# Performance work log

Measured on AMD Instinct MI355X. Metric: run time of the kernel, lower is better.

Reference implementation:

```python
import jax, jax.numpy as jnp
import numpy as np

N0, N1, N2 = 331776, 36864, 4096   # src nodes block0, mid nodes, final items
E0, E1, EP = 294912, 32768, 4096   # edges block0, block1, pos/neg edges
F_RAW, D, H = 128, 256, 512        # raw feat dim, hidden_dims_sum, 2*hidden
N_NODES = 1000000                  # global graph node count (scorer bias)


def setup_inputs() -> dict:
    key = jax.random.key(0)
    ks = jax.random.split(key, 24)
    ri = lambda k, n, hi: jax.random.randint(k, (n,), 0, hi, dtype=jnp.int64 if False else jnp.int32).astype(jnp.int32)
    s = 0.05
    return {
        "feat0": jax.random.normal(ks[0], (N0, F_RAW), jnp.float32),
        "feat_dst": jax.random.normal(ks[1], (N2, F_RAW), jnp.float32),
        "weights0": jax.random.uniform(ks[2], (E0,), jnp.float32),
        "weights1": jax.random.uniform(ks[3], (E1,), jnp.float32),
        "W_proj": jax.random.normal(ks[4], (F_RAW, D), jnp.float32) * s,
        "b_proj": jnp.zeros((D,), jnp.float32),
        "Q1": jax.random.normal(ks[5], (D, H), jnp.float32) * s,
        "bq1": jnp.zeros((H,), jnp.float32),
        "W1": jax.random.normal(ks[6], (D + H, D), jnp.float32) * s,
        "bw1": jnp.zeros((D,), jnp.float32),
        "Q2": jax.random.normal(ks[7], (D, H), jnp.float32) * s,
        "bq2": jnp.zeros((H,), jnp.float32),
        "W2": jax.random.normal(ks[8], (D + H, D), jnp.float32) * s,
        "bw2": jnp.zeros((D,), jnp.float32),
        "bias": jnp.zeros((N_NODES,), jnp.float32),
        "block0_src": ri(ks[9], E0, N0),
        "block0_dst": ri(ks[10], E0, N1),
        "block1_src": ri(ks[11], E1, N1),
        "block1_dst": ri(ks[12], E1, N2),
        "pos_src": ri(ks[13], EP, N2),
        "pos_dst": ri(ks[14], EP, N2),
        "neg_src": ri(ks[15], EP, N2),
        "neg_dst": ri(ks[16], EP, N2),
        "nid": ri(ks[17], N2, N_NODES),
    }


def _l2norm(z):
    n = jnp.linalg.norm(z, axis=1, keepdims=True)
    return z / jnp.where(n == 0, 1.0, n)


def _sage_conv(h_src, h_dst, src, dst, w, Q, bq, W, bw, n_dst):
    # WeightedSAGEConv (dropout omitted: eval-mode deterministic reference)
    n = jax.nn.relu(h_src @ Q + bq)                                   # [N_src, H]
    m = jax.ops.segment_sum(n[src] * w[:, None], dst, num_segments=n_dst)
    ws = jnp.clip(jax.ops.segment_sum(w, dst, num_segments=n_dst), 1.0, None)
    z = jax.nn.relu(jnp.concatenate([m / ws[:, None], h_dst], axis=1) @ W + bw)
    return _l2norm(z)


def _score(h, src, dst, nid, bias):
    # ItemToItemScorer: u_dot_v + src/dst node bias
    return jnp.sum(h[src] * h[dst], axis=1) + bias[nid[src]] + bias[nid[dst]]


def reference(feat0, feat_dst, weights0, weights1, W_proj, b_proj, Q1, bq1, W1, bw1,
              Q2, bq2, W2, bw2, bias, block0_src, block0_dst, block1_src, block1_dst,
              pos_src, pos_dst, neg_src, neg_dst, nid):
    h = feat0 @ W_proj + b_proj                                         # LinearProjector
    h = _sage_conv(h, h[:N1], block0_src, block0_dst, weights0, Q1, bq1, W1, bw1, N1)
    h = _sage_conv(h, h[:N2], block1_src, block1_dst, weights1, Q2, bq2, W2, bw2, N2)
    h_item = (feat_dst @ W_proj + b_proj) + h                           # get_repr skip-add
    pos_score = _score(h_item, pos_src, pos_dst, nid, bias)
    neg_score = _score(h_item, neg_src, neg_dst, nid, bias)
    return (pos_score, neg_score)
```

## Files before the change

kernel.cpp:

```cpp
#include <hip/hip_runtime.h>
#include <hip/hip_bf16.h>

typedef __hip_bfloat16 bf16;
typedef __attribute__((ext_vector_type(8))) short frag8;
typedef __attribute__((ext_vector_type(4))) float f32x4;

#define N0c 331776
#define N1c 36864
#define N2c 4096
#define E0c 294912
#define E1c 32768

__device__ __forceinline__ float bfbits2f(unsigned short b) {
    union { unsigned u; float f; } x; x.u = ((unsigned)b) << 16; return x.f;
}
__device__ __forceinline__ unsigned short f2bfbits(float f) {
    bf16 h = __float2bfloat16(f);
    return *reinterpret_cast<unsigned short*>(&h);
}
__device__ __forceinline__ void load4f(const float* p, float* o) {
    const float4 v = *reinterpret_cast<const float4*>(p);
    o[0] = v.x; o[1] = v.y; o[2] = v.z; o[3] = v.w;
}
__device__ __forceinline__ ushort4 pack4(float4 v) {
    ushort4 o; o.x = f2bfbits(v.x); o.y = f2bfbits(v.y);
    o.z = f2bfbits(v.z); o.w = f2bfbits(v.w); return o;
}
__device__ __forceinline__ void store_c(float* p, float v) { *p = v; }
__device__ __forceinline__ void store_c(bf16* p, float v)  { *p = __float2bfloat16(v); }
__device__ __forceinline__ f32x4 zero4() {
    f32x4 z; z[0] = 0.f; z[1] = 0.f; z[2] = 0.f; z[3] = 0.f; return z;
}
__device__ __forceinline__ f32x4 mfma16(frag8 a, frag8 b, f32x4 c) {
    return __builtin_amdgcn_mfma_f32_16x16x32_bf16(a, b, c, 0, 0, 0);
}

__global__ __launch_bounds__(256) void transpose_bf16(
    const float* __restrict__ src, bf16* __restrict__ dst, int K, int N)
{
    const int idx = blockIdx.x * 256 + threadIdx.x;
    if (idx >= K * N) return;
    const int k = idx / N, n = idx - k * N;
    dst[(size_t)n * K + k] = __float2bfloat16(src[idx]);
}

template<typename TC>
__global__ __launch_bounds__(256) void gemm_mfma_proj(
    const float* __restrict__ A, const bf16* __restrict__ WpT,
    const float* __restrict__ bp, TC* __restrict__ C)
{
    __shared__ bf16 Xs[64 * 136];

    const int tid = threadIdx.x;
    const int lane = tid & 63, wave = tid >> 6;
    const int row0 = blockIdx.x * 64;

    {
        const int r = tid >> 2, q = tid & 3;
        const float* ar = A + (size_t)(row0 + r) * 128 + q * 32;
        bf16* xr = Xs + r * 136 + q * 32;
        #pragma unroll
        for (int i = 0; i < 8; ++i)
            *reinterpret_cast<ushort4*>(xr + i * 4) =
                pack4(*reinterpret_cast<const float4*>(ar + i * 4));
    }
    __syncthreads();

    const int lr = lane & 15;
    const int lk = (lane >> 4) * 8;
    const int lm4 = (lane >> 4) * 4;

    f32x4 acc[4][4];
    #pragma unroll
    for (int mi = 0; mi < 4; ++mi)
        #pragma unroll
        for (int ni = 0; ni < 4; ++ni) acc[mi][ni] = zero4();

    #pragma unroll
    for (int kk = 0; kk < 4; ++kk) {
        frag8 a[4], b[4];
        #pragma unroll
        for (int mi = 0; mi < 4; ++mi)
            a[mi] = *reinterpret_cast<const frag8*>(&Xs[(mi * 16 + lr) * 136 + kk * 32 + lk]);
        #pragma unroll
        for (int ni = 0; ni < 4; ++ni)
            b[ni] = *reinterpret_cast<const frag8*>(
                WpT + (size_t)(wave * 64 + ni * 16 + lr) * 128 + kk * 32 + lk);
        #pragma unroll
        for (int mi = 0; mi < 4; ++mi)
            #pragma unroll
            for (int ni = 0; ni < 4; ++ni)
                acc[mi][ni] = mfma16(a[mi], b[ni], acc[mi][ni]);
    }

    #pragma unroll
    for (int ni = 0; ni < 4; ++ni) {
        const int c = wave * 64 + ni * 16 + lr;
        const float bb = bp[c];
        #pragma unroll
        for (int mi = 0; mi < 4; ++mi)
            #pragma unroll
            for (int i = 0; i < 4; ++i)
                store_c(C + (size_t)(row0 + mi * 16 + lm4 + i) * 256 + c,
                        acc[mi][ni][i] + bb);
    }
}

template<typename TC>
__global__ __launch_bounds__(256) void gemm_mfma_concat(
    const float* __restrict__ m, const float* __restrict__ wsum,
    const bf16* __restrict__ hdst, const bf16* __restrict__ WT,
    const float* __restrict__ bias, TC* __restrict__ C)
{
    __shared__ bf16 As[64 * 136];

    const int tid = threadIdx.x;
    const int lane = tid & 63, wave = tid >> 6;
    const int row0 = blockIdx.x * 64;
    const int r = tid >> 2, q = tid & 3;
    const float inv = 1.f / fmaxf(wsum[row0 + r], 1.f);

    const int lr = lane & 15;
    const int lk = (lane >> 4) * 8;
    const int lm4 = (lane >> 4) * 4;

    f32x4 acc[4][4];
    #pragma unroll
    for (int mi = 0; mi < 4; ++mi)
        #pragma unroll
        for (int ni = 0; ni < 4; ++ni) acc[mi][ni] = zero4();

    #pragma unroll
    for (int ch = 0; ch < 6; ++ch) {
        bf16* xr = As + r * 136 + q * 32;
        if (ch < 4) {
            const float* srcp = m + (size_t)(row0 + r) * 512 + ch * 128 + q * 32;
            #pragma unroll
            for (int i = 0; i < 8; ++i) {
                float4 v = *reinterpret_cast<const float4*>(srcp + i * 4);
                v.x *= inv; v.y *= inv; v.z *= inv; v.w *= inv;
                *reinterpret_cast<ushort4*>(xr + i * 4) = pack4(v);
            }
        } else {
            const bf16* srcp = hdst + (size_t)(row0 + r) * 256 + (ch - 4) * 128 + q * 32;
            #pragma unroll
            for (int i = 0; i < 8; ++i)
                *reinterpret_cast<ushort4*>(xr + i * 4) =
                    *reinterpret_cast<const ushort4*>(srcp + i * 4);
        }
        __syncthreads();

        #pragma unroll
        for (int kk = 0; kk < 4; ++kk) {
            frag8 a[4], b[4];
            #pragma unroll
            for (int mi = 0; mi < 4; ++mi)
                a[mi] = *reinterpret_cast<const frag8*>(&As[(mi * 16 + lr) * 136 + kk * 32 + lk]);
            #pragma unroll
            for (int ni = 0; ni < 4; ++ni)
                b[ni] = *reinterpret_cast<const frag8*>(
                    WT + (size_t)(wave * 64 + ni * 16 + lr) * 768 + ch * 128 + kk * 32 + lk);
            #pragma unroll
            for (int mi = 0; mi < 4; ++mi)
                #pragma unroll
                for (int ni = 0; ni < 4; ++ni)
                    acc[mi][ni] = mfma16(a[mi], b[ni], acc[mi][ni]);
        }
        __syncthreads();
    }

    #pragma unroll
    for (int ni = 0; ni < 4; ++ni) {
        const int c = wave * 64 + ni * 16 + lr;
        const float bb = bias[c];
        #pragma unroll
        for (int mi = 0; mi < 4; ++mi)
            #pragma unroll
            for (int i = 0; i < 4; ++i)
                store_c(C + (size_t)(row0 + mi * 16 + lm4 + i) * 256 + c,
                        fmaxf(acc[mi][ni][i] + bb, 0.f));
    }
}

__global__ __launch_bounds__(256) void edge1_mfma(
    const float* __restrict__ feat0, const bf16* __restrict__ WpT,
    const float* __restrict__ bp, const bf16* __restrict__ Q1T,
    const float* __restrict__ bq1,
    const int* __restrict__ src, const int* __restrict__ dst,
    const float* __restrict__ w,
    float* __restrict__ mout, float* __restrict__ wsum)
{
    __shared__ bf16 Xs[64 * 136];
    __shared__ bf16 Hs[64 * 264];
    __shared__ int   dsts[64];
    __shared__ float wts[64];

    const int tid = threadIdx.x;
    const int lane = tid & 63, wave = tid >> 6;
    const size_t e0 = (size_t)blockIdx.x * 64;

    if (tid < 64) { dsts[tid] = dst[e0 + tid]; wts[tid] = w[e0 + tid]; }

    {
        const int r = tid >> 2, q = tid & 3;
        const int s = src[e0 + r];
        const float* fr = feat0 + (size_t)s * 128 + q * 32;
        bf16* xr = Xs + r * 136 + q * 32;
        #pragma unroll
        for (int i = 0; i < 8; ++i)
            *reinterpret_cast<ushort4*>(xr + i * 4) =
                pack4(*reinterpret_cast<const float4*>(fr + i * 4));
    }
    __syncthreads();

    const int lr = lane & 15;
    const int lk = (lane >> 4) * 8;
    const int lm4 = (lane >> 4) * 4;

    {
        f32x4 acc[4][4];
        #pragma unroll
        for (int mi = 0; mi < 4; ++mi)
            #pragma unroll
            for (int ni = 0; ni < 4; ++ni) acc[mi][ni] = zero4();

        #pragma unroll
        for (int kk = 0; kk < 4; ++kk) {
            frag8 a[4], b[4];
            #pragma unroll
            for (int mi = 0; mi < 4; ++mi)
                a[mi] = *reinterpret_cast<const frag8*>(&Xs[(mi * 16 + lr) * 136 + kk * 32 + lk]);
            #pragma unroll
            for (int ni = 0; ni < 4; ++ni)
                b[ni] = *reinterpret_cast<const frag8*>(
                    WpT + (size_t)(wave * 64 + ni * 16 + lr) * 128 + kk * 32 + lk);
            #pragma unroll
            for (int mi = 0; mi < 4; ++mi)
                #pragma unroll
                for (int ni = 0; ni < 4; ++ni)
                    acc[mi][ni] = mfma16(a[mi], b[ni], acc[mi][ni]);
        }
        #pragma unroll
        for (int ni = 0; ni < 4; ++ni) {
            const int c = wave * 64 + ni * 16 + lr;
            const float bb = bp[c];
            #pragma unroll
            for (int mi = 0; mi < 4; ++mi)
                #pragma unroll
                for (int i = 0; i < 4; ++i)
                    Hs[(mi * 16 + lm4 + i) * 264 + c] =
                        __float2bfloat16(acc[mi][ni][i] + bb);
        }
    }
    __syncthreads();

    #pragma unroll
    for (int pass = 0; pass < 2; ++pass) {
        const int nc0 = wave * 128 + pass * 64;
        f32x4 acc[4][4];
        #pragma unroll
        for (int mi = 0; mi < 4; ++mi)
            #pragma unroll
            for (int ni = 0; ni < 4; ++ni) acc[mi][ni] = zero4();

        #pragma unroll
        for (int kk = 0; kk < 8; ++kk) {
            frag8 a[4], b[4];
            #pragma unroll
            for (int mi = 0; mi < 4; ++mi)
                a[mi] = *reinterpret_cast<const frag8*>(&Hs[(mi * 16 + lr) * 264 + kk * 32 + lk]);
            #pragma unroll
            for (int ni = 0; ni < 4; ++ni)
                b[ni] = *reinterpret_cast<const frag8*>(
                    Q1T + (size_t)(nc0 + ni * 16 + lr) * 256 + kk * 32 + lk);
            #pragma unroll
            for (int mi = 0; mi < 4; ++mi)
                #pragma unroll
                for (int ni = 0; ni < 4; ++ni)
                    acc[mi][ni] = mfma16(a[mi], b[ni], acc[mi][ni]);
        }
        #pragma unroll
        for (int ni = 0; ni < 4; ++ni) {
            const int c = nc0 + ni * 16 + lr;
            const float bb = bq1[c];
            #pragma unroll
            for (int mi = 0; mi < 4; ++mi)
                #pragma unroll
                for (int i = 0; i < 4; ++i) {
                    const int row = mi * 16 + lm4 + i;
                    const float val = fmaxf(acc[mi][ni][i] + bb, 0.f) * wts[row];
                    atomicAdd(&mout[(size_t)dsts[row] * 512 + c], val);
                }
        }
    }
    if (tid < 64) atomicAdd(&wsum[dsts[tid]], wts[tid]);
}

__global__ __launch_bounds__(256) void edge2_mfma(
    const bf16* __restrict__ zn, const bf16* __restrict__ Q2T,
    const float* __restrict__ bq2,
    const int* __restrict__ src, const int* __restrict__ dst,
    const float* __restrict__ w,
    float* __restrict__ mout, float* __restrict__ wsum)
{
    __shared__ bf16 Zs[64 * 264];
    __shared__ int   dsts[64];
    __shared__ float wts[64];

    const int tid = threadIdx.x;
    const int lane = tid & 63, wave = tid >> 6;
    const size_t e0 = (size_t)blockIdx.x * 64;

    if (tid < 64) { dsts[tid] = dst[e0 + tid]; wts[tid] = w[e0 + tid]; }

    {
        const int r = tid >> 2, q = tid & 3;
        const int s = src[e0 + r];
        const bf16* zr = zn + (size_t)s * 256 + q * 64;
        bf16* zo = Zs + r * 264 + q * 64;
        #pragma unroll
        for (int i = 0; i < 16; ++i)
            *reinterpret_cast<ushort4*>(zo + i * 4) =
                *reinterpret_cast<const ushort4*>(zr + i * 4);
    }
    __syncthreads();

    const int lr = lane & 15;
    const int lk = (lane >> 4) * 8;
    const int lm4 = (lane >> 4) * 4;

    #pragma unroll
    for (int pass = 0; pass < 2; ++pass) {
        const int nc0 = wave * 128 + pass * 64;
        f32x4 acc[4][4];
        #pragma unroll
        for (int mi = 0; mi < 4; ++mi)
            #pragma unroll
            for (int ni = 0; ni < 4; ++ni) acc[mi][ni] = zero4();

        #pragma unroll
        for (int kk = 0; kk < 8; ++kk) {
            frag8 a[4], b[4];
            #pragma unroll
            for (int mi = 0; mi < 4; ++mi)
                a[mi] = *reinterpret_cast<const frag8*>(&Zs[(mi * 16 + lr) * 264 + kk * 32 + lk]);
            #pragma unroll
            for (int ni = 0; ni < 4; ++ni)
                b[ni] = *reinterpret_cast<const frag8*>(
                    Q2T + (size_t)(nc0 + ni * 16 + lr) * 256 + kk * 32 + lk);
            #pragma unroll
            for (int mi = 0; mi < 4; ++mi)
                #pragma unroll
                for (int ni = 0; ni < 4; ++ni)
                    acc[mi][ni] = mfma16(a[mi], b[ni], acc[mi][ni]);
        }
        #pragma unroll
        for (int ni = 0; ni < 4; ++ni) {
            const int c = nc0 + ni * 16 + lr;
            const float bb = bq2[c];
            #pragma unroll
            for (int mi = 0; mi < 4; ++mi)
                #pragma unroll
                for (int i = 0; i < 4; ++i) {
                    const int row = mi * 16 + lm4 + i;
                    const float val = fmaxf(acc[mi][ni][i] + bb, 0.f) * wts[row];
                    atomicAdd(&mout[(size_t)dsts[row] * 512 + c], val);
                }
        }
    }
    if (tid < 64) atomicAdd(&wsum[dsts[tid]], wts[tid]);
}

__global__ __launch_bounds__(256) void l2norm_kernel(
    const bf16* __restrict__ Z, bf16* __restrict__ out, int rows)
{
    const int wave = threadIdx.x >> 6, lane = threadIdx.x & 63;
    const int row = blockIdx.x * 4 + wave;
    if (row >= rows) return;
    const ushort4 u = *reinterpret_cast<const ushort4*>(Z + (size_t)row * 256 + lane * 4);
    float v[4] = { bfbits2f(u.x), bfbits2f(u.y), bfbits2f(u.z), bfbits2f(u.w) };
    float ss = v[0]*v[0] + v[1]*v[1] + v[2]*v[2] + v[3]*v[3];
    #pragma unroll
    for (int off = 32; off; off >>= 1) ss += __shfl_xor(ss, off, 64);
    const float scale = (ss == 0.f) ? 1.f : (1.f / sqrtf(ss));
    ushort4 o;
    o.x = f2bfbits(v[0]*scale); o.y = f2bfbits(v[1]*scale);
    o.z = f2bfbits(v[2]*scale); o.w = f2bfbits(v[3]*scale);
    *reinterpret_cast<ushort4*>(out + (size_t)row * 256 + lane * 4) = o;
}

__global__ __launch_bounds__(256) void l2norm_add_kernel(
    const float* __restrict__ Z, const float* __restrict__ P,
    float* __restrict__ out, int rows)
{
    const int wave = threadIdx.x >> 6, lane = threadIdx.x & 63;
    const int row = blockIdx.x * 4 + wave;
    if (row >= rows) return;
    float v[4];
    load4f(Z + (size_t)row * 256 + lane * 4, v);
    float ss = v[0]*v[0] + v[1]*v[1] + v[2]*v[2] + v[3]*v[3];
    #pragma unroll
    for (int off = 32; off; off >>= 1) ss += __shfl_xor(ss, off, 64);
    const float scale = (ss == 0.f) ? 1.f : (1.f / sqrtf(ss));
    float p[4];
    load4f(P + (size_t)row * 256 + lane * 4, p);
    float4 o;
    o.x = p[0] + v[0]*scale; o.y = p[1] + v[1]*scale;
    o.z = p[2] + v[2]*scale; o.w = p[3] + v[3]*scale;
    *reinterpret_cast<float4*>(out + (size_t)row * 256 + lane * 4) = o;
}

__global__ __launch_bounds__(256) void score_kernel(
    const float* __restrict__ h,
    const int* __restrict__ ps, const int* __restrict__ pdi,
    const int* __restrict__ ns, const int* __restrict__ nd,
    const int* __restrict__ nid, const float* __restrict__ bias,
    float* __restrict__ out)
{
    const int wave = threadIdx.x >> 6, lane = threadIdx.x & 63;
    const int e = blockIdx.x * 4 + wave;
    const int ei = e & 4095;
    const int s = (e < 4096) ? ps[ei] : ns[ei];
    const int d = (e < 4096) ? pdi[ei] : nd[ei];
    float a[4], b[4];
    load4f(h + (size_t)s * 256 + lane * 4, a);
    load4f(h + (size_t)d * 256 + lane * 4, b);
    float dot = a[0]*b[0] + a[1]*b[1] + a[2]*b[2] + a[3]*b[3];
    #pragma unroll
    for (int off = 32; off; off >>= 1) dot += __shfl_xor(dot, off, 64);
    if (lane == 0)
        out[e] = dot + bias[nid[s]] + bias[nid[d]];
}

extern "C" void kernel_launch(void* const* d_in, const int* in_sizes, int n_in,
                              void* d_out, int out_size, void* d_ws, size_t ws_size,
                              hipStream_t stream)
{
    const float* feat0    = (const float*)d_in[0];
    const float* feat_dst = (const float*)d_in[1];
    const float* weights0 = (const float*)d_in[2];
    const float* weights1 = (const float*)d_in[3];
    const float* W_proj   = (const float*)d_in[4];
    const float* b_proj   = (const float*)d_in[5];
    const float* Q1       = (const float*)d_in[6];
    const float* bq1      = (const float*)d_in[7];
    const float* W1       = (const float*)d_in[8];
    const float* bw1      = (const float*)d_in[9];
    const float* Q2       = (const float*)d_in[10];
    const float* bq2      = (const float*)d_in[11];
    const float* W2       = (const float*)d_in[12];
    const float* bw2      = (const float*)d_in[13];
    const float* biasN    = (const float*)d_in[14];
    const int* b0s = (const int*)d_in[15];
    const int* b0d = (const int*)d_in[16];
    const int* b1s = (const int*)d_in[17];
    const int* b1d = (const int*)d_in[18];
    const int* pos_src = (const int*)d_in[19];
    const int* pos_dst = (const int*)d_in[20];
    const int* neg_src = (const int*)d_in[21];
    const int* neg_dst = (const int*)d_in[22];
    const int* nid     = (const int*)d_in[23];

    char* ws = (char*)d_ws;
    size_t off = 0;
    auto alloc = [&](size_t bytes) -> void* {
        void* p = ws + off; off += (bytes + 255) & ~(size_t)255; return p;
    };
    float* m1    = (float*)alloc((size_t)N1c * 512 * 4);
    bf16*  h1dst = (bf16*) alloc((size_t)N1c * 256 * 2);
    bf16*  z1b   = (bf16*) alloc((size_t)N1c * 256 * 2);
    float* ws0   = (float*)alloc((size_t)N1c * 4);
    bf16*  WpT   = (bf16*) alloc((size_t)256 * 128 * 2);
    bf16*  Q1T   = (bf16*) alloc((size_t)512 * 256 * 2);
    bf16*  Q2T   = (bf16*) alloc((size_t)512 * 256 * 2);
    bf16*  W1T   = (bf16*) alloc((size_t)256 * 768 * 2);
    bf16*  W2T   = (bf16*) alloc((size_t)256 * 768 * 2);

    char* r1 = (char*)m1;
    float* m2     = (float*)r1;
    float* ws1    = (float*)(r1 + (size_t)N2c * 512 * 4);
    float* z2     = (float*)(r1 + (size_t)N2c * 512 * 4 + 65536);
    float* pdbuf  = z2 + (size_t)N2c * 256;
    float* h_item = pdbuf + (size_t)N2c * 256;
    bf16* z1n = h1dst;

    transpose_bf16<<<(128*256 + 255)/256, 256, 0, stream>>>(W_proj, WpT, 128, 256);
    transpose_bf16<<<(256*512 + 255)/256, 256, 0, stream>>>(Q1, Q1T, 256, 512);
    transpose_bf16<<<(256*512 + 255)/256, 256, 0, stream>>>(Q2, Q2T, 256, 512);
    transpose_bf16<<<(768*256 + 255)/256, 256, 0, stream>>>(W1, W1T, 768, 256);
    transpose_bf16<<<(768*256 + 255)/256, 256, 0, stream>>>(W2, W2T, 768, 256);

    hipMemsetAsync(m1,  0, (size_t)N1c * 512 * 4, stream);
    hipMemsetAsync(ws0, 0, (size_t)N1c * 4,       stream);

    gemm_mfma_proj<bf16><<<N1c/64, 256, 0, stream>>>(feat0, WpT, b_proj, h1dst);

    edge1_mfma<<<E0c/64, 256, 0, stream>>>(
        feat0, WpT, b_proj, Q1T, bq1, b0s, b0d, weights0, m1, ws0);

    gemm_mfma_concat<bf16><<<N1c/64, 256, 0, stream>>>(
        m1, ws0, h1dst, W1T, bw1, z1b);

    l2norm_kernel<<<N1c/4, 256, 0, stream>>>(z1b, z1n, N1c);

    hipMemsetAsync(m2,  0, (size_t)N2c * 512 * 4, stream);
    hipMemsetAsync(ws1, 0, (size_t)N2c * 4,       stream);

    edge2_mfma<<<E1c/64, 256, 0, stream>>>(
        z1n, Q2T, bq2, b1s, b1d, weights1, m2, ws1);

    gemm_mfma_concat<float><<<N2c/64, 256, 0, stream>>>(
        m2, ws1, z1n, W2T, bw2, z2);

    gemm_mfma_proj<float><<<N2c/64, 256, 0, stream>>>(feat_dst, WpT, b_proj, pdbuf);

    l2norm_add_kernel<<<N2c/4, 256, 0, stream>>>(z2, pdbuf, h_item, N2c);

    score_kernel<<<2048, 256, 0, stream>>>(
        h_item, pos_src, pos_dst, neg_src, neg_dst, nid, biasN, (float*)d_out);
}
```

Measured before the change: 741.5 us.

## Replace atomic scatter aggregation with CSR sort-by-destination and segmented reduction

Builds a destination-sorted permutation (histogram, scan, fill) for each block's edges. The edge kernels now write per-edge bf16 messages to a buffer, and a per-destination reduce kernel sums them and divides by the weight sum, which replaces the float atomics into m. Layer 1 now projects all N0 source nodes once with a GEMM instead of recomputing the projection for every edge. The cost is a large per-edge message buffer, a single-block scan, extra launches, and bf16 rounding of the messages and the mean.

```diff
diff --git a/kernel.cpp b/kernel.cpp
--- a/kernel.cpp
+++ b/kernel.cpp
@@ -44,6 +44,48 @@
     dst[(size_t)n * K + k] = __float2bfloat16(src[idx]);
 }
 
+__global__ __launch_bounds__(256) void hist_kernel(
+    const int* __restrict__ dst, int* __restrict__ cnt, int E)
+{
+    const int e = blockIdx.x * 256 + threadIdx.x;
+    if (e < E) atomicAdd(&cnt[dst[e]], 1);
+}
+
+__global__ __launch_bounds__(256) void scan_kernel(
+    const int* __restrict__ cnt, int* __restrict__ base, int n)
+{
+    __shared__ int ps[256];
+    const int t = threadIdx.x;
+    const int chunk = (n + 255) >> 8;
+    const int lo = t * chunk;
+    const int hi = (lo + chunk < n) ? lo + chunk : n;
+    int s = 0;
+    for (int i = lo; i < hi; ++i) s += cnt[i];
+    ps[t] = s;
+    __syncthreads();
+    for (int off = 1; off < 256; off <<= 1) {
+        int v = (t >= off) ? ps[t - off] : 0;
+        __syncthreads();
+        ps[t] += v;
+        __syncthreads();
+    }
+    int run = ps[t] - s;
+    for (int i = lo; i < hi; ++i) { base[i] = run; run += cnt[i]; }
+    if (t == 255) base[n] = ps[255];
+}
+
+__global__ __launch_bounds__(256) void fill_kernel(
+    const int* __restrict__ dst, const int* __restrict__ base,
+    int* __restrict__ cursor, int* __restrict__ perm, int E)
+{
+    const int e = blockIdx.x * 256 + threadIdx.x;
+    if (e < E) {
+        const int d = dst[e];
+        const int p = base[d] + atomicAdd(&cursor[d], 1);
+        perm[p] = e;
+    }
+}
+
 template<typename TC>
 __global__ __launch_bounds__(256) void gemm_mfma_proj(
     const float* __restrict__ A, const bf16* __restrict__ WpT,
@@ -106,11 +148,113 @@
     }
 }
 
+__global__ __launch_bounds__(256) void edge_csr(
+    const bf16* __restrict__ zn, const bf16* __restrict__ QT,
+    const float* __restrict__ bq,
+    const int* __restrict__ perm, const int* __restrict__ src,
+    const float* __restrict__ w,
+    bf16* __restrict__ nbuf)
+{
+    __shared__ bf16 Zs[64 * 264];
+    __shared__ int   srcs[64];
+    __shared__ float wts[64];
+
+    const int tid = threadIdx.x;
+    const int lane = tid & 63, wave = tid >> 6;
+    const size_t p0 = (size_t)blockIdx.x * 64;
+
+    if (tid < 64) {
+        const int e = perm[p0 + tid];
+        srcs[tid] = src[e];
+        wts[tid]  = w[e];
+    }
+    __syncthreads();
+
+    {
+        const int r = tid >> 2, q = tid & 3;
+        const bf16* zr = zn + (size_t)srcs[r] * 256 + q * 64;
+        bf16* zo = Zs + r * 264 + q * 64;
+        #pragma unroll
+        for (int i = 0; i < 16; ++i)
+            *reinterpret_cast<ushort4*>(zo + i * 4) =
+                *reinterpret_cast<const ushort4*>(zr + i * 4);
+    }
+    __syncthreads();
+
+    const int lr = lane & 15;
+    const int lk = (lane >> 4) * 8;
+    const int lm4 = (lane >> 4) * 4;
+
+    #pragma unroll
+    for (int pass = 0; pass < 2; ++pass) {
+        const int nc0 = wave * 128 + pass * 64;
+        f32x4 acc[4][4];
+        #pragma unroll
+        for (int mi = 0; mi < 4; ++mi)
+            #pragma unroll
+            for (int ni = 0; ni < 4; ++ni) acc[mi][ni] = zero4();
+
+        #pragma unroll
+        for (int kk = 0; kk < 8; ++kk) {
+            frag8 a[4], b[4];
+            #pragma unroll
+            for (int mi = 0; mi < 4; ++mi)
+                a[mi] = *reinterpret_cast<const frag8*>(&Zs[(mi * 16 + lr) * 264 + kk * 32 + lk]);
+            #pragma unroll
+            for (int ni = 0; ni < 4; ++ni)
+                b[ni] = *reinterpret_cast<const frag8*>(
+                    QT + (size_t)(nc0 + ni * 16 + lr) * 256 + kk * 32 + lk);
+            #pragma unroll
+            for (int mi = 0; mi < 4; ++mi)
+                #pragma unroll
+                for (int ni = 0; ni < 4; ++ni)
+                    acc[mi][ni] = mfma16(a[mi], b[ni], acc[mi][ni]);
+        }
+        #pragma unroll
+        for (int ni = 0; ni < 4; ++ni) {
+            const int c = nc0 + ni * 16 + lr;
+            const float bb = bq[c];
+            #pragma unroll
+            for (int mi = 0; mi < 4; ++mi)
+                #pragma unroll
+                for (int i = 0; i < 4; ++i) {
+                    const int row = mi * 16 + lm4 + i;
+                    const float val = fmaxf(acc[mi][ni][i] + bb, 0.f) * wts[row];
+                    nbuf[(p0 + row) * 512 + c] = __float2bfloat16(val);
+                }
+        }
+    }
+}
+
+__global__ __launch_bounds__(256) void reduce_csr(
+    const bf16* __restrict__ nbuf, const int* __restrict__ base,
+    const int* __restrict__ perm, const float* __restrict__ w,
+    bf16* __restrict__ mout)
+{
+    const int d = blockIdx.x;
+    const int lo = base[d], hi = base[d + 1];
+    __shared__ float s_inv;
+    if (threadIdx.x == 0) {
+        float s = 0.f;
+        for (int k = lo; k < hi; ++k) s += w[perm[k]];
+        s_inv = 1.f / fmaxf(s, 1.f);
+    }
+    __syncthreads();
+    const int c = threadIdx.x * 2;
+    float a0 = 0.f, a1 = 0.f;
+    for (int k = lo; k < hi; ++k) {
+        const ushort2 u = *reinterpret_cast<const ushort2*>(nbuf + (size_t)k * 512 + c);
+        a0 += bfbits2f(u.x); a1 += bfbits2f(u.y);
+    }
+    ushort2 o; o.x = f2bfbits(a0 * s_inv); o.y = f2bfbits(a1 * s_inv);
+    *reinterpret_cast<ushort2*>(mout + (size_t)d * 512 + c) = o;
+}
+
 template<typename TC>
 __global__ __launch_bounds__(256) void gemm_mfma_concat(
-    const float* __restrict__ m, const float* __restrict__ wsum,
-    const bf16* __restrict__ hdst, const bf16* __restrict__ WT,
-    const float* __restrict__ bias, TC* __restrict__ C)
+    const bf16* __restrict__ m, const bf16* __restrict__ hdst,
+    const bf16* __restrict__ WT, const float* __restrict__ bias,
+    TC* __restrict__ C)
 {
     __shared__ bf16 As[64 * 136];
 
@@ -118,7 +262,6 @@
     const int lane = tid & 63, wave = tid >> 6;
     const int row0 = blockIdx.x * 64;
     const int r = tid >> 2, q = tid & 3;
-    const float inv = 1.f / fmaxf(wsum[row0 + r], 1.f);
 
     const int lr = lane & 15;
     const int lk = (lane >> 4) * 8;
@@ -133,21 +276,13 @@
     #pragma unroll
     for (int ch = 0; ch < 6; ++ch) {
         bf16* xr = As + r * 136 + q * 32;
-        if (ch < 4) {
-            const float* srcp = m + (size_t)(row0 + r) * 512 + ch * 128 + q * 32;
-            #pragma unroll
-            for (int i = 0; i < 8; ++i) {
-                float4 v = *reinterpret_cast<const float4*>(srcp + i * 4);
-                v.x *= inv; v.y *= inv; v.z *= inv; v.w *= inv;
-                *reinterpret_cast<ushort4*>(xr + i * 4) = pack4(v);
-            }
-        } else {
-            const bf16* srcp = hdst + (size_t)(row0 + r) * 256 + (ch - 4) * 128 + q * 32;
-            #pragma unroll
-            for (int i = 0; i < 8; ++i)
-                *reinterpret_cast<ushort4*>(xr + i * 4) =
-                    *reinterpret_cast<const ushort4*>(srcp + i * 4);
-        }
+        const bf16* srcp = (ch < 4)
+            ? m    + (size_t)(row0 + r) * 512 + ch * 128 + q * 32
+            : hdst + (size_t)(row0 + r) * 256 + (ch - 4) * 128 + q * 32;
+        #pragma unroll
+        for (int i = 0; i < 8; ++i)
+            *reinterpret_cast<ushort4*>(xr + i * 4) =
+                *reinterpret_cast<const ushort4*>(srcp + i * 4);
         __syncthreads();
 
         #pragma unroll
@@ -180,195 +315,6 @@
                 store_c(C + (size_t)(row0 + mi * 16 + lm4 + i) * 256 + c,
                         fmaxf(acc[mi][ni][i] + bb, 0.f));
     }
-}
-
-__global__ __launch_bounds__(256) void edge1_mfma(
-    const float* __restrict__ feat0, const bf16* __restrict__ WpT,
-    const float* __restrict__ bp, const bf16* __restrict__ Q1T,
-    const float* __restrict__ bq1,
-    const int* __restrict__ src, const int* __restrict__ dst,
-    const float* __restrict__ w,
-    float* __restrict__ mout, float* __restrict__ wsum)
-{
-    __shared__ bf16 Xs[64 * 136];
-    __shared__ bf16 Hs[64 * 264];
-    __shared__ int   dsts[64];
-    __shared__ float wts[64];
-
-    const int tid = threadIdx.x;
-    const int lane = tid & 63, wave = tid >> 6;
-    const size_t e0 = (size_t)blockIdx.x * 64;
-
-    if (tid < 64) { dsts[tid] = dst[e0 + tid]; wts[tid] = w[e0 + tid]; }
-
-    {
-        const int r = tid >> 2, q = tid & 3;
-        const int s = src[e0 + r];
-        const float* fr = feat0 + (size_t)s * 128 + q * 32;
-        bf16* xr = Xs + r * 136 + q * 32;
-        #pragma unroll
-        for (int i = 0; i < 8; ++i)
-            *reinterpret_cast<ushort4*>(xr + i * 4) =
-                pack4(*reinterpret_cast<const float4*>(fr + i * 4));
-    }
-    __syncthreads();
-
-    const int lr = lane & 15;
-    const int lk = (lane >> 4) * 8;
-    const int lm4 = (lane >> 4) * 4;
-
-    {
-        f32x4 acc[4][4];
-        #pragma unroll
-        for (int mi = 0; mi < 4; ++mi)
-            #pragma unroll
-            for (int ni = 0; ni < 4; ++ni) acc[mi][ni] = zero4();
-
-        #pragma unroll
-        for (int kk = 0; kk < 4; ++kk) {
-            frag8 a[4], b[4];
-            #pragma unroll
-            for (int mi = 0; mi < 4; ++mi)
-                a[mi] = *reinterpret_cast<const frag8*>(&Xs[(mi * 16 + lr) * 136 + kk * 32 + lk]);
-            #pragma unroll
-            for (int ni = 0; ni < 4; ++ni)
-                b[ni] = *reinterpret_cast<const frag8*>(
-                    WpT + (size_t)(wave * 64 + ni * 16 + lr) * 128 + kk * 32 + lk);
-            #pragma unroll
-            for (int mi = 0; mi < 4; ++mi)
-                #pragma unroll
-                for (int ni = 0; ni < 4; ++ni)
-                    acc[mi][ni] = mfma16(a[mi], b[ni], acc[mi][ni]);
-        }
-        #pragma unroll
-        for (int ni = 0; ni < 4; ++ni) {
-            const int c = wave * 64 + ni * 16 + lr;
-            const float bb = bp[c];
-            #pragma unroll
-            for (int mi = 0; mi < 4; ++mi)
-                #pragma unroll
-                for (int i = 0; i < 4; ++i)
-                    Hs[(mi * 16 + lm4 + i) * 264 + c] =
-                        __float2bfloat16(acc[mi][ni][i] + bb);
-        }
-    }
-    __syncthreads();
-
-    #pragma unroll
-    for (int pass = 0; pass < 2; ++pass) {
-        const int nc0 = wave * 128 + pass * 64;
-        f32x4 acc[4][4];
-        #pragma unroll
-        for (int mi = 0; mi < 4; ++mi)
-            #pragma unroll
-            for (int ni = 0; ni < 4; ++ni) acc[mi][ni] = zero4();
-
-        #pragma unroll
-        for (int kk = 0; kk < 8; ++kk) {
-            frag8 a[4], b[4];
-            #pragma unroll
-            for (int mi = 0; mi < 4; ++mi)
-                a[mi] = *reinterpret_cast<const frag8*>(&Hs[(mi * 16 + lr) * 264 + kk * 32 + lk]);
-            #pragma unroll
-            for (int ni = 0; ni < 4; ++ni)
-                b[ni] = *reinterpret_cast<const frag8*>(
-                    Q1T + (size_t)(nc0 + ni * 16 + lr) * 256 + kk * 32 + lk);
-            #pragma unroll
-            for (int mi = 0; mi < 4; ++mi)
-                #pragma unroll
-                for (int ni = 0; ni < 4; ++ni)
-                    acc[mi][ni] = mfma16(a[mi], b[ni], acc[mi][ni]);
-        }
-        #pragma unroll
-        for (int ni = 0; ni < 4; ++ni) {
-            const int c = nc0 + ni * 16 + lr;
-            const float bb = bq1[c];
-            #pragma unroll
-            for (int mi = 0; mi < 4; ++mi)
-                #pragma unroll
-                for (int i = 0; i < 4; ++i) {
-                    const int row = mi * 16 + lm4 + i;
-                    const float val = fmaxf(acc[mi][ni][i] + bb, 0.f) * wts[row];
-                    atomicAdd(&mout[(size_t)dsts[row] * 512 + c], val);
-                }
-        }
-    }
-    if (tid < 64) atomicAdd(&wsum[dsts[tid]], wts[tid]);
-}
-
-__global__ __launch_bounds__(256) void edge2_mfma(
-    const bf16* __restrict__ zn, const bf16* __restrict__ Q2T,
-    const float* __restrict__ bq2,
-    const int* __restrict__ src, const int* __restrict__ dst,
-    const float* __restrict__ w,
-    float* __restrict__ mout, float* __restrict__ wsum)
-{
-    __shared__ bf16 Zs[64 * 264];
-    __shared__ int   dsts[64];
-    __shared__ float wts[64];
-
-    const int tid = threadIdx.x;
-    const int lane = tid & 63, wave = tid >> 6;
-    const size_t e0 = (size_t)blockIdx.x * 64;
-
-    if (tid < 64) { dsts[tid] = dst[e0 + tid]; wts[tid] = w[e0 + tid]; }
-
-    {
-        const int r = tid >> 2, q = tid & 3;
-        const int s = src[e0 + r];
-        const bf16* zr = zn + (size_t)s * 256 + q * 64;
-        bf16* zo = Zs + r * 264 + q * 64;
-        #pragma unroll
-        for (int i = 0; i < 16; ++i)
-            *reinterpret_cast<ushort4*>(zo + i * 4) =
-                *reinterpret_cast<const ushort4*>(zr + i * 4);
-    }
-    __syncthreads();
-
-    const int lr = lane & 15;
-    const int lk = (lane >> 4) * 8;
-    const int lm4 = (lane >> 4) * 4;
-
-    #pragma unroll
-    for (int pass = 0; pass < 2; ++pass) {
-        const int nc0 = wave * 128 + pass * 64;
-        f32x4 acc[4][4];
-        #pragma unroll
-        for (int mi = 0; mi < 4; ++mi)
-            #pragma unroll
-            for (int ni = 0; ni < 4; ++ni) acc[mi][ni] = zero4();
-
-        #pragma unroll
-        for (int kk = 0; kk < 8; ++kk) {
-            frag8 a[4], b[4];
-            #pragma unroll
-            for (int mi = 0; mi < 4; ++mi)
-                a[mi] = *reinterpret_cast<const frag8*>(&Zs[(mi * 16 + lr) * 264 + kk * 32 + lk]);
-            #pragma unroll
-            for (int ni = 0; ni < 4; ++ni)
-                b[ni] = *reinterpret_cast<const frag8*>(
-                    Q2T + (size_t)(nc0 + ni * 16 + lr) * 256 + kk * 32 + lk);
-            #pragma unroll
-            for (int mi = 0; mi < 4; ++mi)
-                #pragma unroll
-                for (int ni = 0; ni < 4; ++ni)
-                    acc[mi][ni] = mfma16(a[mi], b[ni], acc[mi][ni]);
-        }
-        #pragma unroll
-        for (int ni = 0; ni < 4; ++ni) {
-            const int c = nc0 + ni * 16 + lr;
-            const float bb = bq2[c];
-            #pragma unroll
-            for (int mi = 0; mi < 4; ++mi)
-                #pragma unroll
-                for (int i = 0; i < 4; ++i) {
-                    const int row = mi * 16 + lm4 + i;
-                    const float val = fmaxf(acc[mi][ni][i] + bb, 0.f) * wts[row];
-                    atomicAdd(&mout[(size_t)dsts[row] * 512 + c], val);
-                }
-        }
-    }
-    if (tid < 64) atomicAdd(&wsum[dsts[tid]], wts[tid]);
 }
 
 __global__ __launch_bounds__(256) void l2norm_kernel(
@@ -466,23 +412,27 @@
     auto alloc = [&](size_t bytes) -> void* {
         void* p = ws + off; off += (bytes + 255) & ~(size_t)255; return p;
     };
-    float* m1    = (float*)alloc((size_t)N1c * 512 * 4);
-    bf16*  h1dst = (bf16*) alloc((size_t)N1c * 256 * 2);
-    bf16*  z1b   = (bf16*) alloc((size_t)N1c * 256 * 2);
-    float* ws0   = (float*)alloc((size_t)N1c * 4);
-    bf16*  WpT   = (bf16*) alloc((size_t)256 * 128 * 2);
-    bf16*  Q1T   = (bf16*) alloc((size_t)512 * 256 * 2);
-    bf16*  Q2T   = (bf16*) alloc((size_t)512 * 256 * 2);
-    bf16*  W1T   = (bf16*) alloc((size_t)256 * 768 * 2);
-    bf16*  W2T   = (bf16*) alloc((size_t)256 * 768 * 2);
-
-    char* r1 = (char*)m1;
-    float* m2     = (float*)r1;
-    float* ws1    = (float*)(r1 + (size_t)N2c * 512 * 4);
-    float* z2     = (float*)(r1 + (size_t)N2c * 512 * 4 + 65536);
-    float* pdbuf  = z2 + (size_t)N2c * 256;
-    float* h_item = pdbuf + (size_t)N2c * 256;
-    bf16* z1n = h1dst;
+    bf16* h0    = (bf16*)alloc((size_t)N0c * 256 * 2);
+    char* r2    = (char*)alloc((size_t)E0c * 512 * 2);
+    bf16* m1    = (bf16*)alloc((size_t)N1c * 512 * 2);
+    bf16* WpT   = (bf16*)alloc((size_t)256 * 128 * 2);
+    bf16* Q1T   = (bf16*)alloc((size_t)512 * 256 * 2);
+    bf16* Q2T   = (bf16*)alloc((size_t)512 * 256 * 2);
+    bf16* W1T   = (bf16*)alloc((size_t)256 * 768 * 2);
+    bf16* W2T   = (bf16*)alloc((size_t)256 * 768 * 2);
+    int*  cnt    = (int*)alloc((size_t)(N1c + 1) * 4);
+    int*  base   = (int*)alloc((size_t)(N1c + 1) * 4);
+    int*  cursor = (int*)alloc((size_t)N1c * 4);
+    int*  perm   = (int*)alloc((size_t)E0c * 4);
+
+    bf16* nbuf1 = (bf16*)r2;
+    bf16* z1b   = (bf16*)r2;
+    bf16* z1n   = (bf16*)(r2 + 18874368);
+    bf16* nbuf2 = (bf16*)(r2 + 37748736);
+    bf16* m2    = (bf16*)(r2 + 71303168);
+    float* z2     = (float*)(r2 + 75497472);
+    float* pdbuf  = (float*)(r2 + 79691776);
+    float* h_item = (float*)(r2 + 83886080);
 
     transpose_bf16<<<(128*256 + 255)/256, 256, 0, stream>>>(W_proj, WpT, 128, 256);
     transpose_bf16<<<(256*512 + 255)/256, 256, 0, stream>>>(Q1, Q1T, 256, 512);
@@ -490,27 +440,33 @@
     transpose_bf16<<<(768*256 + 255)/256, 256, 0, stream>>>(W1, W1T, 768, 256);
     transpose_bf16<<<(768*256 + 255)/256, 256, 0, stream>>>(W2, W2T, 768, 256);
 
-    hipMemsetAsync(m1,  0, (size_t)N1c * 512 * 4, stream);
-    hipMemsetAsync(ws0, 0, (size_t)N1c * 4,       stream);
-
-    gemm_mfma_proj<bf16><<<N1c/64, 256, 0, stream>>>(feat0, WpT, b_proj, h1dst);
-
-    edge1_mfma<<<E0c/64, 256, 0, stream>>>(
-        feat0, WpT, b_proj, Q1T, bq1, b0s, b0d, weights0, m1, ws0);
-
-    gemm_mfma_concat<bf16><<<N1c/64, 256, 0, stream>>>(
-        m1, ws0, h1dst, W1T, bw1, z1b);
+    gemm_mfma_proj<bf16><<<N0c/64, 256, 0, stream>>>(feat0, WpT, b_proj, h0);
+
+    hipMemsetAsync(cnt,    0, (size_t)N1c * 4, stream);
+    hipMemsetAsync(cursor, 0, (size_t)N1c * 4, stream);
+    hist_kernel<<<E0c/256, 256, 0, stream>>>(b0d, cnt, E0c);
+    scan_kernel<<<1, 256, 0, stream>>>(cnt, base, N1c);
+    fill_kernel<<<E0c/256, 256, 0, stream>>>(b0d, base, cursor, perm, E0c);
+
+    edge_csr<<<E0c/64, 256, 0, stream>>>(h0, Q1T, bq1, perm, b0s, weights0, nbuf1);
+
+    reduce_csr<<<N1c, 256, 0, stream>>>(nbuf1, base, perm, weights0, m1);
+
+    gemm_mfma_concat<bf16><<<N1c/64, 256, 0, stream>>>(m1, h0, W1T, bw1, z1b);
 
     l2norm_kernel<<<N1c/4, 256, 0, stream>>>(z1b, z1n, N1c);
 
-    hipMemsetAsync(m2,  0, (size_t)N2c * 512 * 4, stream);
-    hipMemsetAsync(ws1, 0, (size_t)N2c * 4,       stream);
-
-    edge2_mfma<<<E1c/64, 256, 0, stream>>>(
-        z1n, Q2T, bq2, b1s, b1d, weights1, m2, ws1);
-
-    gemm_mfma_concat<float><<<N2c/64, 256, 0, stream>>>(
-        m2, ws1, z1n, W2T, bw2, z2);
+    hipMemsetAsync(cnt,    0, (size_t)N2c * 4, stream);
+    hipMemsetAsync(cursor, 0, (size_t)N2c * 4, stream);
+    hist_kernel<<<E1c/256, 256, 0, stream>>>(b1d, cnt, E1c);
+    scan_kernel<<<1, 256, 0, stream>>>(cnt, base, N2c);
+    fill_kernel<<<E1c/256, 256, 0, stream>>>(b1d, base, cursor, perm, E1c);
+
+    edge_csr<<<E1c/64, 256, 0, stream>>>(z1n, Q2T, bq2, perm, b1s, weights1, nbuf2);
+
+    reduce_csr<<<N2c, 256, 0, stream>>>(nbuf2, base, perm, weights1, m2);
+
+    gemm_mfma_concat<float><<<N2c/64, 256, 0, stream>>>(m2, z1n, W2T, bw2, z2);
 
     gemm_mfma_proj<float><<<N2c/64, 256, 0, stream>>>(feat_dst, WpT, b_proj, pdbuf);
 
```

Result: slower. 793.0 us (+6.9%).
